# Optimization experiments

Hardware: AMD Instinct MI355X
Metric: run time of the kernel (lower is better)

Reference implementation:

```python
import jax, jax.numpy as jnp
import numpy as np

B, T, D, H, M, CM = 8, 4096, 512, 8, 64, 4
E = D // H          # head dim = 64
F = T // 2 + 1      # rfft length = 2049


def setup_inputs() -> dict:
    key = jax.random.key(0)
    ks = jax.random.split(key, 6)
    scale = 1.0 / (E * E)  # FEDformer weight init: scale * rand
    return {
        "x": jax.random.normal(ks[0], (B, T, D), jnp.float32),
        "Wp": jax.random.normal(ks[1], (D, D), jnp.float32) * (D ** -0.5),
        "bp": jnp.zeros((D,), jnp.float32),
        "w_real": jax.random.uniform(ks[2], (H, E, E, M), jnp.float32) * scale,
        "w_imag": jax.random.uniform(ks[3], (H, E, E, M), jnp.float32) * scale,
        "W1": jax.random.normal(ks[4], (CM * D, D), jnp.float32) * (D ** -0.5),
        "W2": jax.random.normal(ks[5], (D, CM * D), jnp.float32) * ((CM * D) ** -0.5),
        "mode_index": jnp.arange(M, dtype=jnp.int32),  # mode_selection='lowest'
    }


def reference(x, Wp, bp, w_real, w_imag, W1, W2, mode_index):
    b, t, d = x.shape
    # SingleMultiheadProjection: Linear(D, D) then split heads -> [B,T,H,E]
    q = (x @ Wp + bp).reshape(b, t, H, E)
    # FEBf (FourierBlock): permute to [B,H,E,T], rfft over time
    xh = jnp.transpose(q, (0, 2, 3, 1))            # [B,H,E,T]
    x_ft = jnp.fft.rfft(xh, axis=-1)               # [B,H,E,F] complex64
    # sparse mode gather + per-mode complex mixing (bhi,hio->bho per mode)
    xm = jnp.take(x_ft, mode_index, axis=-1)       # [B,H,E,M]
    w = w_real + 1j * w_imag                       # [H,E,E,M]
    om = jnp.einsum('bhim,hiom->bhom', xm, w)      # [B,H,E,M]
    # scatter selected modes back into the zeroed spectrum, inverse transform
    out_ft = jnp.zeros((b, H, E, F), dtype=x_ft.dtype).at[..., mode_index].set(om)
    attn = jnp.fft.irfft(out_ft, n=t, axis=-1)     # [B,H,E,T]
    attn = jnp.transpose(attn, (0, 3, 1, 2)).reshape(b, t, d)
    # residual (dropout=0 / eval mode)
    x = x + attn
    # pointwise-conv FFN: Conv1d(k=1, bias=False) == GEMM over channels
    y = jax.nn.relu(jnp.einsum('btd,cd->btc', x, W1))   # [B,T,CM*D]
    y = jnp.einsum('btc,dc->btd', y, W2)                # [B,T,D]
    return x + y
```

## Files before the change

kernel.cpp:

```cpp
#include <hip/hip_runtime.h>
#include <hip/hip_bf16.h>


#define T_LEN 4096
#define D_MODEL 512
#define NB 8
#define NH 8
#define NE 64
#define NM 64
#define DFF 2048
#define NROWS (NB * T_LEN)
#define NK 128
#define TSPLIT 8
#define TCH (T_LEN / TSPLIT)

typedef __attribute__((ext_vector_type(8))) short bf16x8;
typedef __attribute__((ext_vector_type(4))) float f32x4;

__device__ inline ushort f2bf_rne(float f) {
    unsigned u = __float_as_uint(f);
    unsigned r = u + 0x7FFFu + ((u >> 16) & 1u);
    return (ushort)(r >> 16);
}
__device__ inline float bf2f(ushort h) { return __uint_as_float(((unsigned)h) << 16); }
__device__ inline void split_bf16(float v, ushort& h, ushort& l) {
    h = f2bf_rne(v);
    l = f2bf_rne(v - bf2f(h));
}

#define GLOAD16(gp, lp)                                                            \
    __builtin_amdgcn_global_load_lds(                                              \
        (const __attribute__((address_space(1))) void*)(gp),                       \
        (__attribute__((address_space(3))) void*)(lp), 16, 0, 0)

__global__ __launch_bounds__(256) void basis_kernel(float* __restrict__ basis) {
    int idx = blockIdx.x * 256 + threadIdx.x;
    int t = idx >> 6, m = idx & 63;
    int r = (t * m) & (T_LEN - 1);
    float ang = (float)r * 1.5339807878856412e-3f;
    float s, c;
    sincosf(ang, &s, &c);
    basis[t * 128 + 2 * m]     = c;
    basis[t * 128 + 2 * m + 1] = s;
}

__global__ __launch_bounds__(256) void decomp_kernel(const float* __restrict__ in,
                                                     ushort* __restrict__ hi,
                                                     ushort* __restrict__ lo, int n4) {
    int i = blockIdx.x * 256 + threadIdx.x;
    if (i >= n4) return;
    float4 v = ((const float4*)in)[i];
    ushort4 h, l;
    split_bf16(v.x, h.x, l.x);
    split_bf16(v.y, h.y, l.y);
    split_bf16(v.z, h.z, l.z);
    split_bf16(v.w, h.w, l.w);
    ((ushort4*)hi)[i] = h;
    ((ushort4*)lo)[i] = l;
}

__global__ __launch_bounds__(256) void dft2_kernel(const float* __restrict__ x,
                                                   const float* __restrict__ basis,
                                                   float* __restrict__ pp) {
    __shared__ float xs[64][68];
    __shared__ float bs[64][132];
    int d0 = blockIdx.x * 64;
    int b  = blockIdx.y;
    int tc = blockIdx.z;
    int t0 = tc * TCH;
    int tid = threadIdx.x;
    int tx = tid & 15, ty = tid >> 4;
    float4 acc0[4] = {};
    float4 acc1[4] = {};

    for (int tt = 0; tt < TCH; tt += 64) {
        const float* xrow = x + ((size_t)b * T_LEN + t0 + tt) * D_MODEL + d0;
#pragma unroll
        for (int l = 0; l < 4; ++l) {
            int f = (tid + l * 256) * 4;
            int r = f >> 6, c = f & 63;
            *(float4*)&xs[r][c] = *(const float4*)(xrow + (size_t)r * D_MODEL + c);
        }
        const float* brow = basis + (size_t)(t0 + tt) * NK;
#pragma unroll
        for (int l = 0; l < 8; ++l) {
            int f = (tid + l * 256) * 4;
            int r = f >> 7, c = f & 127;
            *(float4*)&bs[r][c] = *(const float4*)(brow + (size_t)r * NK + c);
        }
        __syncthreads();
#pragma unroll 4
        for (int t = 0; t < 64; ++t) {
            float4 xv = *(const float4*)&xs[t][ty * 4];
            float4 b0 = *(const float4*)&bs[t][tx * 4];
            float4 b1 = *(const float4*)&bs[t][tx * 4 + 64];
            float xa[4] = {xv.x, xv.y, xv.z, xv.w};
#pragma unroll
            for (int di = 0; di < 4; ++di) {
                acc0[di].x = fmaf(xa[di], b0.x, acc0[di].x);
                acc0[di].y = fmaf(xa[di], b0.y, acc0[di].y);
                acc0[di].z = fmaf(xa[di], b0.z, acc0[di].z);
                acc0[di].w = fmaf(xa[di], b0.w, acc0[di].w);
                acc1[di].x = fmaf(xa[di], b1.x, acc1[di].x);
                acc1[di].y = fmaf(xa[di], b1.y, acc1[di].y);
                acc1[di].z = fmaf(xa[di], b1.z, acc1[di].z);
                acc1[di].w = fmaf(xa[di], b1.w, acc1[di].w);
            }
        }
        __syncthreads();
    }
#pragma unroll
    for (int di = 0; di < 4; ++di) {
        int d = d0 + ty * 4 + di;
        size_t base = (((size_t)tc * NB + b) * D_MODEL + d) * NK;
        *(float4*)(pp + base + tx * 4)      = acc0[di];
        *(float4*)(pp + base + 64 + tx * 4) = acc1[di];
    }
}

__global__ __launch_bounds__(256) void dft_reduce_kernel(const float* __restrict__ pp,
                                                         float* __restrict__ Xm) {
    int idx = blockIdx.x * 256 + threadIdx.x;
    const size_t stride = (size_t)NB * D_MODEL * NK;
    float s = 0.f;
#pragma unroll
    for (int tc = 0; tc < TSPLIT; ++tc) s += pp[(size_t)tc * stride + idx];
    Xm[idx] = (idx & 1) ? -s : s;
}

__global__ __launch_bounds__(512) void proj_kernel(const float* __restrict__ Xm,
                                                   const float* __restrict__ Wp,
                                                   const float* __restrict__ bpv,
                                                   float* __restrict__ qm) {
    int m = blockIdx.x, b = blockIdx.y;
    int c = threadIdx.x;
    float qr = 0.f, qi = 0.f;
#pragma unroll 4
    for (int d = 0; d < D_MODEL; ++d) {
        float2 xv = *(const float2*)(Xm + ((size_t)(b * D_MODEL + d) * NM + m) * 2);
        float w = Wp[(size_t)d * D_MODEL + c];
        qr = fmaf(xv.x, w, qr);
        qi = fmaf(xv.y, w, qi);
    }
    if (m == 0) qr += bpv[c] * (float)T_LEN;
    size_t o = ((size_t)(b * D_MODEL + c) * NM + m) * 2;
    qm[o] = qr; qm[o + 1] = qi;
}

__global__ __launch_bounds__(64) void mix_kernel(const float* __restrict__ qm,
                                                 const float* __restrict__ wre,
                                                 const float* __restrict__ wim,
                                                 float* __restrict__ omB) {
    int o = blockIdx.x, h = blockIdx.y, m = threadIdx.x;
    float ar[NB], ai[NB];
#pragma unroll
    for (int b = 0; b < NB; ++b) { ar[b] = 0.f; ai[b] = 0.f; }
    for (int i = 0; i < NE; ++i) {
        size_t wo = (((size_t)(h * NE + i) * NE + o) * NM) + m;
        float wr = wre[wo], wi = wim[wo];
#pragma unroll
        for (int b = 0; b < NB; ++b) {
            float2 q = *(const float2*)(qm + ((size_t)(b * D_MODEL + h * NE + i) * NM + m) * 2);
            ar[b] = fmaf(q.x, wr, fmaf(-q.y, wi, ar[b]));
            ai[b] = fmaf(q.x, wi, fmaf(q.y, wr, ai[b]));
        }
    }
    float cm = (m == 0) ? (1.0f / T_LEN) : (2.0f / T_LEN);
    int cidx = h * NE + o;
#pragma unroll
    for (int b = 0; b < NB; ++b) {
        omB[((size_t)b * 128 + 2 * m) * D_MODEL + cidx]     = ar[b] * cm;
        omB[((size_t)b * 128 + 2 * m + 1) * D_MODEL + cidx] = (m == 0) ? 0.f : -ai[b] * cm;
    }
}

__global__ __launch_bounds__(256) void idft_kernel(const float* __restrict__ x,
                                                   const float* __restrict__ basis,
                                                   const float* __restrict__ omB,
                                                   ushort* __restrict__ xh_hi,
                                                   ushort* __restrict__ xh_lo,
                                                   float* __restrict__ out) {
    __shared__ float bs[64][129];
    __shared__ float os[128][65];
    int b = blockIdx.z;
    int tt = blockIdx.y * 64;
    int dd = blockIdx.x * 64;
    int tid = threadIdx.x;
    for (int i = tid; i < 64 * 128; i += 256) {
        int r = i >> 7, k = i & 127;
        bs[r][k] = basis[(size_t)(tt + r) * 128 + k];
    }
    for (int i = tid; i < 128 * 64; i += 256) {
        int k = i >> 6, dl = i & 63;
        os[k][dl] = omB[((size_t)b * 128 + k) * D_MODEL + dd + dl];
    }
    __syncthreads();
    int tx = tid & 15, ty = tid >> 4;
    int r0 = ty * 4, c0 = tx * 4;
    float acc[4][4] = {};
#pragma unroll 4
    for (int k = 0; k < 128; ++k) {
        float a[4], bv[4];
#pragma unroll
        for (int i = 0; i < 4; ++i) a[i] = bs[r0 + i][k];
#pragma unroll
        for (int j = 0; j < 4; ++j) bv[j] = os[k][c0 + j];
#pragma unroll
        for (int i = 0; i < 4; ++i)
#pragma unroll
            for (int j = 0; j < 4; ++j) acc[i][j] = fmaf(a[i], bv[j], acc[i][j]);
    }
#pragma unroll
    for (int i = 0; i < 4; ++i) {
        size_t off = ((size_t)b * T_LEN + tt + r0 + i) * D_MODEL + dd + c0;
        float4 xv = *(const float4*)(x + off);
        float4 o4;
        o4.x = xv.x + acc[i][0]; o4.y = xv.y + acc[i][1];
        o4.z = xv.z + acc[i][2]; o4.w = xv.w + acc[i][3];
        *(float4*)(out + off) = o4;
        ushort4 hv, lv;
        split_bf16(o4.x, hv.x, lv.x);
        split_bf16(o4.y, hv.y, lv.y);
        split_bf16(o4.z, hv.z, lv.z);
        split_bf16(o4.w, hv.w, lv.w);
        *(ushort4*)(xh_hi + off) = hv;
        *(ushort4*)(xh_lo + off) = lv;
    }
}


__global__ __launch_bounds__(256) void ffn1_mfma(const ushort* __restrict__ Ag_h,
                                                 const ushort* __restrict__ Ag_l,
                                                 const ushort* __restrict__ Bg_h,
                                                 const ushort* __restrict__ Bg_l,
                                                 ushort* __restrict__ Yh,
                                                 ushort* __restrict__ Yl,
                                                 int co, int CH) {
    __shared__ ushort Ah[128][32], Al[128][32], Bh[128][32], Bl[128][32];
    int rr = blockIdx.y * 128;
    int ccl = blockIdx.x * 128;
    int cc = co + ccl;
    int tid = threadIdx.x;
    int lane = tid & 63, w = tid >> 6;
    int wr = (w >> 1) * 64, wc = (w & 1) * 64;
    f32x4 acc[4][4] = {};
    int c0 = w * 2;
    int srow = c0 * 16 + (lane >> 2);
    int koff = (lane & 3) * 8;

    for (int kk = 0; kk < D_MODEL; kk += 32) {
        GLOAD16(Ag_h + (size_t)(rr + srow) * D_MODEL + kk + koff, &Ah[c0 * 16][0]);
        GLOAD16(Ag_h + (size_t)(rr + srow + 16) * D_MODEL + kk + koff, &Ah[c0 * 16 + 16][0]);
        GLOAD16(Ag_l + (size_t)(rr + srow) * D_MODEL + kk + koff, &Al[c0 * 16][0]);
        GLOAD16(Ag_l + (size_t)(rr + srow + 16) * D_MODEL + kk + koff, &Al[c0 * 16 + 16][0]);
        GLOAD16(Bg_h + (size_t)(cc + srow) * D_MODEL + kk + koff, &Bh[c0 * 16][0]);
        GLOAD16(Bg_h + (size_t)(cc + srow + 16) * D_MODEL + kk + koff, &Bh[c0 * 16 + 16][0]);
        GLOAD16(Bg_l + (size_t)(cc + srow) * D_MODEL + kk + koff, &Bl[c0 * 16][0]);
        GLOAD16(Bg_l + (size_t)(cc + srow + 16) * D_MODEL + kk + koff, &Bl[c0 * 16 + 16][0]);
        __syncthreads();
        int arow = wr + (lane & 15);
        int kq = (lane >> 4) * 8;
        bf16x8 afh[4], afl[4];
#pragma unroll
        for (int i = 0; i < 4; ++i) {
            afh[i] = *(const bf16x8*)&Ah[arow + i * 16][kq];
            afl[i] = *(const bf16x8*)&Al[arow + i * 16][kq];
        }
#pragma unroll
        for (int j = 0; j < 4; ++j) {
            int brow = wc + j * 16 + (lane & 15);
            bf16x8 bfh = *(const bf16x8*)&Bh[brow][kq];
            bf16x8 bfl = *(const bf16x8*)&Bl[brow][kq];
#pragma unroll
            for (int i = 0; i < 4; ++i) {
                acc[i][j] = __builtin_amdgcn_mfma_f32_16x16x32_bf16(afh[i], bfh, acc[i][j], 0, 0, 0);
                acc[i][j] = __builtin_amdgcn_mfma_f32_16x16x32_bf16(afl[i], bfh, acc[i][j], 0, 0, 0);
                acc[i][j] = __builtin_amdgcn_mfma_f32_16x16x32_bf16(afh[i], bfl, acc[i][j], 0, 0, 0);
            }
        }
        __syncthreads();
    }
#pragma unroll
    for (int i = 0; i < 4; ++i) {
        int row = rr + wr + i * 16 + (lane >> 4) * 4;
#pragma unroll
        for (int j = 0; j < 4; ++j) {
            int col = ccl + wc + j * 16 + (lane & 15);
#pragma unroll
            for (int q = 0; q < 4; ++q) {
                float v = fmaxf(acc[i][j][q], 0.f);
                ushort h, l;
                split_bf16(v, h, l);
                size_t o = (size_t)(row + q) * CH + col;
                Yh[o] = h;
                Yl[o] = l;
            }
        }
    }
}

__global__ __launch_bounds__(256) void ffn2_mfma(const ushort* __restrict__ Ag_h,
                                                 const ushort* __restrict__ Ag_l,
                                                 const ushort* __restrict__ Bg_h,
                                                 const ushort* __restrict__ Bg_l,
                                                 float* __restrict__ out,
                                                 int co, int CH) {
    __shared__ ushort Ah[128][32], Al[128][32], Bh[128][32], Bl[128][32];
    int rr = blockIdx.y * 128;
    int dd = blockIdx.x * 128;
    int tid = threadIdx.x;
    int lane = tid & 63, w = tid >> 6;
    int wr = (w >> 1) * 64, wc = (w & 1) * 64;
    f32x4 acc[4][4] = {};
    int c0 = w * 2;
    int srow = c0 * 16 + (lane >> 2);
    int koff = (lane & 3) * 8;

    for (int kk = 0; kk < CH; kk += 32) {
        GLOAD16(Ag_h + (size_t)(rr + srow) * CH + kk + koff, &Ah[c0 * 16][0]);
        GLOAD16(Ag_h + (size_t)(rr + srow + 16) * CH + kk + koff, &Ah[c0 * 16 + 16][0]);
        GLOAD16(Ag_l + (size_t)(rr + srow) * CH + kk + koff, &Al[c0 * 16][0]);
        GLOAD16(Ag_l + (size_t)(rr + srow + 16) * CH + kk + koff, &Al[c0 * 16 + 16][0]);
        GLOAD16(Bg_h + (size_t)(dd + srow) * DFF + co + kk + koff, &Bh[c0 * 16][0]);
        GLOAD16(Bg_h + (size_t)(dd + srow + 16) * DFF + co + kk + koff, &Bh[c0 * 16 + 16][0]);
        GLOAD16(Bg_l + (size_t)(dd + srow) * DFF + co + kk + koff, &Bl[c0 * 16][0]);
        GLOAD16(Bg_l + (size_t)(dd + srow + 16) * DFF + co + kk + koff, &Bl[c0 * 16 + 16][0]);
        __syncthreads();
        int arow = wr + (lane & 15);
        int kq = (lane >> 4) * 8;
        bf16x8 afh[4], afl[4];
#pragma unroll
        for (int i = 0; i < 4; ++i) {
            afh[i] = *(const bf16x8*)&Ah[arow + i * 16][kq];
            afl[i] = *(const bf16x8*)&Al[arow + i * 16][kq];
        }
#pragma unroll
        for (int j = 0; j < 4; ++j) {
            int brow = wc + j * 16 + (lane & 15);
            bf16x8 bfh = *(const bf16x8*)&Bh[brow][kq];
            bf16x8 bfl = *(const bf16x8*)&Bl[brow][kq];
#pragma unroll
            for (int i = 0; i < 4; ++i) {
                acc[i][j] = __builtin_amdgcn_mfma_f32_16x16x32_bf16(afh[i], bfh, acc[i][j], 0, 0, 0);
                acc[i][j] = __builtin_amdgcn_mfma_f32_16x16x32_bf16(afl[i], bfh, acc[i][j], 0, 0, 0);
                acc[i][j] = __builtin_amdgcn_mfma_f32_16x16x32_bf16(afh[i], bfl, acc[i][j], 0, 0, 0);
            }
        }
        __syncthreads();
    }
#pragma unroll
    for (int i = 0; i < 4; ++i) {
        int row = rr + wr + i * 16 + (lane >> 4) * 4;
#pragma unroll
        for (int j = 0; j < 4; ++j) {
            int col = dd + wc + j * 16 + (lane & 15);
#pragma unroll
            for (int q = 0; q < 4; ++q) {
                size_t o = (size_t)(row + q) * D_MODEL + col;
                out[o] += acc[i][j][q];
            }
        }
    }
}

extern "C" void kernel_launch(void* const* d_in, const int* in_sizes, int n_in,
                              void* d_out, int out_size, void* d_ws, size_t ws_size,
                              hipStream_t stream) {
    const float* x   = (const float*)d_in[0];
    const float* Wp  = (const float*)d_in[1];
    const float* bpv = (const float*)d_in[2];
    const float* wre = (const float*)d_in[3];
    const float* wim = (const float*)d_in[4];
    const float* W1  = (const float*)d_in[5];
    const float* W2  = (const float*)d_in[6];
    float* out = (float*)d_out;

    char* ws = (char*)d_ws;
    const size_t MB = (size_t)1 << 20;
    float*  basis = (float*)(ws + 0 * MB);
    float*  Xm    = (float*)(ws + 2 * MB);
    float*  qm    = (float*)(ws + 4 * MB);
    float*  omB   = (float*)(ws + 6 * MB);
    ushort* w1h   = (ushort*)(ws + 8 * MB);
    ushort* w1l   = (ushort*)(ws + 10 * MB);
    ushort* w2h   = (ushort*)(ws + 12 * MB);
    ushort* w2l   = (ushort*)(ws + 14 * MB);
    ushort* xh_hi = (ushort*)(ws + 16 * MB);
    ushort* xh_lo = (ushort*)(ws + 48 * MB);
    char*   y1b   = ws + 80 * MB;
    float*  pp    = (float*)(ws + 16 * MB);

    size_t avail = (ws_size > 80 * MB) ? ws_size - 80 * MB : 0;
    int CH = 2048;
    while (CH > 128 && (size_t)NROWS * CH * 2 * sizeof(ushort) > avail) CH >>= 1;
    ushort* y1h = (ushort*)y1b;
    ushort* y1l = (ushort*)(y1b + (size_t)NROWS * CH * sizeof(ushort));

    basis_kernel<<<1024, 256, 0, stream>>>(basis);
    decomp_kernel<<<1024, 256, 0, stream>>>(W1, w1h, w1l, DFF * D_MODEL / 4);
    decomp_kernel<<<1024, 256, 0, stream>>>(W2, w2h, w2l, DFF * D_MODEL / 4);
    dft2_kernel<<<dim3(8, 8, TSPLIT), 256, 0, stream>>>(x, basis, pp);
    dft_reduce_kernel<<<(NB * D_MODEL * NK) / 256, 256, 0, stream>>>(pp, Xm);
    proj_kernel<<<dim3(64, 8), 512, 0, stream>>>(Xm, Wp, bpv, qm);
    mix_kernel<<<dim3(64, 8), 64, 0, stream>>>(qm, wre, wim, omB);
    idft_kernel<<<dim3(8, 64, 8), 256, 0, stream>>>(x, basis, omB, xh_hi, xh_lo, out);
    for (int co = 0; co < DFF; co += CH) {
        ffn1_mfma<<<dim3(CH / 128, NROWS / 128), 256, 0, stream>>>(
            xh_hi, xh_lo, w1h, w1l, y1h, y1l, co, CH);
        ffn2_mfma<<<dim3(D_MODEL / 128, NROWS / 128), 256, 0, stream>>>(
            y1h, y1l, w2h, w2l, out, co, CH);
    }
}
```

Baseline: 869.8 us.

## Rework DFT split, mix/idft parallelism, and FFN GEMM K-step with XCD swizzle

Doubles the time split of the forward DFT and gives the mode-mixing kernel one block per batch, so each thread handles one batch. A transposed basis is added so the inverse-DFT kernel can load tiles with float4 and read them from padded shared memory without strided access. Both FFN MFMA GEMMs now stage 64 K-elements per barrier in a two-slot shared buffer and launch on a 1-D grid whose block index is remapped across the 8 XCDs. The intent is fewer barriers, better L2 locality and higher parallelism in the small kernels. The cost is double the shared memory per GEMM block and an extra 2 MB basis buffer.

```diff
diff --git a/kernel.cpp b/kernel.cpp
--- a/kernel.cpp
+++ b/kernel.cpp
@@ -11,7 +11,7 @@
 #define DFF 2048
 #define NROWS (NB * T_LEN)
 #define NK 128
-#define TSPLIT 8
+#define TSPLIT 16
 #define TCH (T_LEN / TSPLIT)
 
 typedef __attribute__((ext_vector_type(8))) short bf16x8;
@@ -33,15 +33,18 @@
         (const __attribute__((address_space(1))) void*)(gp),                       \
         (__attribute__((address_space(3))) void*)(lp), 16, 0, 0)
 
-__global__ __launch_bounds__(256) void basis_kernel(float* __restrict__ basis) {
+__global__ __launch_bounds__(256) void basis_kernel(float* __restrict__ basis,
+                                                    float* __restrict__ basisT) {
     int idx = blockIdx.x * 256 + threadIdx.x;
-    int t = idx >> 6, m = idx & 63;
+    int k = idx >> 12, t = idx & 4095;
+    int m = k >> 1;
     int r = (t * m) & (T_LEN - 1);
     float ang = (float)r * 1.5339807878856412e-3f;
     float s, c;
     sincosf(ang, &s, &c);
-    basis[t * 128 + 2 * m]     = c;
-    basis[t * 128 + 2 * m + 1] = s;
+    float v = (k & 1) ? s : c;
+    basisT[(size_t)k * T_LEN + t] = v;
+    basis[(size_t)t * NK + k]    = v;
 }
 
 __global__ __launch_bounds__(256) void decomp_kernel(const float* __restrict__ in,
@@ -151,72 +154,63 @@
                                                  const float* __restrict__ wre,
                                                  const float* __restrict__ wim,
                                                  float* __restrict__ omB) {
-    int o = blockIdx.x, h = blockIdx.y, m = threadIdx.x;
-    float ar[NB], ai[NB];
-#pragma unroll
-    for (int b = 0; b < NB; ++b) { ar[b] = 0.f; ai[b] = 0.f; }
+    int o = blockIdx.x, h = blockIdx.y, b = blockIdx.z, m = threadIdx.x;
+    float ar = 0.f, ai = 0.f;
     for (int i = 0; i < NE; ++i) {
         size_t wo = (((size_t)(h * NE + i) * NE + o) * NM) + m;
         float wr = wre[wo], wi = wim[wo];
-#pragma unroll
-        for (int b = 0; b < NB; ++b) {
-            float2 q = *(const float2*)(qm + ((size_t)(b * D_MODEL + h * NE + i) * NM + m) * 2);
-            ar[b] = fmaf(q.x, wr, fmaf(-q.y, wi, ar[b]));
-            ai[b] = fmaf(q.x, wi, fmaf(q.y, wr, ai[b]));
-        }
+        float2 q = *(const float2*)(qm + ((size_t)(b * D_MODEL + h * NE + i) * NM + m) * 2);
+        ar = fmaf(q.x, wr, fmaf(-q.y, wi, ar));
+        ai = fmaf(q.x, wi, fmaf(q.y, wr, ai));
     }
     float cm = (m == 0) ? (1.0f / T_LEN) : (2.0f / T_LEN);
     int cidx = h * NE + o;
-#pragma unroll
-    for (int b = 0; b < NB; ++b) {
-        omB[((size_t)b * 128 + 2 * m) * D_MODEL + cidx]     = ar[b] * cm;
-        omB[((size_t)b * 128 + 2 * m + 1) * D_MODEL + cidx] = (m == 0) ? 0.f : -ai[b] * cm;
-    }
-}
-
-__global__ __launch_bounds__(256) void idft_kernel(const float* __restrict__ x,
-                                                   const float* __restrict__ basis,
-                                                   const float* __restrict__ omB,
-                                                   ushort* __restrict__ xh_hi,
-                                                   ushort* __restrict__ xh_lo,
-                                                   float* __restrict__ out) {
-    __shared__ float bs[64][129];
-    __shared__ float os[128][65];
-    int b = blockIdx.z;
+    omB[((size_t)b * 128 + 2 * m) * D_MODEL + cidx]     = ar * cm;
+    omB[((size_t)b * 128 + 2 * m + 1) * D_MODEL + cidx] = (m == 0) ? 0.f : -ai * cm;
+}
+
+__global__ __launch_bounds__(256) void idft2_kernel(const float* __restrict__ x,
+                                                    const float* __restrict__ basisT,
+                                                    const float* __restrict__ omB,
+                                                    ushort* __restrict__ xh_hi,
+                                                    ushort* __restrict__ xh_lo,
+                                                    float* __restrict__ out) {
+    __shared__ float bT[128][68];
+    __shared__ float os[128][68];
+    int dd = blockIdx.x * 64;
     int tt = blockIdx.y * 64;
-    int dd = blockIdx.x * 64;
+    int b  = blockIdx.z;
     int tid = threadIdx.x;
-    for (int i = tid; i < 64 * 128; i += 256) {
-        int r = i >> 7, k = i & 127;
-        bs[r][k] = basis[(size_t)(tt + r) * 128 + k];
-    }
-    for (int i = tid; i < 128 * 64; i += 256) {
-        int k = i >> 6, dl = i & 63;
-        os[k][dl] = omB[((size_t)b * 128 + k) * D_MODEL + dd + dl];
+#pragma unroll
+    for (int l = 0; l < 8; ++l) {
+        int f = (tid + l * 256) * 4;
+        int r = f >> 6, c = f & 63;
+        *(float4*)&bT[r][c] = *(const float4*)(basisT + (size_t)r * T_LEN + tt + c);
+        *(float4*)&os[r][c] = *(const float4*)(omB + ((size_t)b * NK + r) * D_MODEL + dd + c);
     }
     __syncthreads();
     int tx = tid & 15, ty = tid >> 4;
-    int r0 = ty * 4, c0 = tx * 4;
-    float acc[4][4] = {};
+    float4 acc[4] = {};
 #pragma unroll 4
     for (int k = 0; k < 128; ++k) {
-        float a[4], bv[4];
-#pragma unroll
-        for (int i = 0; i < 4; ++i) a[i] = bs[r0 + i][k];
-#pragma unroll
-        for (int j = 0; j < 4; ++j) bv[j] = os[k][c0 + j];
-#pragma unroll
-        for (int i = 0; i < 4; ++i)
-#pragma unroll
-            for (int j = 0; j < 4; ++j) acc[i][j] = fmaf(a[i], bv[j], acc[i][j]);
+        float4 av = *(const float4*)&bT[k][ty * 4];
+        float4 bv = *(const float4*)&os[k][tx * 4];
+        float aa[4] = {av.x, av.y, av.z, av.w};
+#pragma unroll
+        for (int i = 0; i < 4; ++i) {
+            acc[i].x = fmaf(aa[i], bv.x, acc[i].x);
+            acc[i].y = fmaf(aa[i], bv.y, acc[i].y);
+            acc[i].z = fmaf(aa[i], bv.z, acc[i].z);
+            acc[i].w = fmaf(aa[i], bv.w, acc[i].w);
+        }
     }
 #pragma unroll
     for (int i = 0; i < 4; ++i) {
-        size_t off = ((size_t)b * T_LEN + tt + r0 + i) * D_MODEL + dd + c0;
+        size_t off = ((size_t)b * T_LEN + tt + ty * 4 + i) * D_MODEL + dd + tx * 4;
         float4 xv = *(const float4*)(x + off);
         float4 o4;
-        o4.x = xv.x + acc[i][0]; o4.y = xv.y + acc[i][1];
-        o4.z = xv.z + acc[i][2]; o4.w = xv.w + acc[i][3];
+        o4.x = xv.x + acc[i].x; o4.y = xv.y + acc[i].y;
+        o4.z = xv.z + acc[i].z; o4.w = xv.w + acc[i].w;
         *(float4*)(out + off) = o4;
         ushort4 hv, lv;
         split_bf16(o4.x, hv.x, lv.x);
@@ -235,10 +229,14 @@
                                                  const ushort* __restrict__ Bg_l,
                                                  ushort* __restrict__ Yh,
                                                  ushort* __restrict__ Yl,
-                                                 int co, int CH) {
-    __shared__ ushort Ah[128][32], Al[128][32], Bh[128][32], Bl[128][32];
-    int rr = blockIdx.y * 128;
-    int ccl = blockIdx.x * 128;
+                                                 int co, int CH, int nx) {
+    __shared__ ushort Ah[2][128][32], Al[2][128][32], Bh[2][128][32], Bl[2][128][32];
+    int nwg = gridDim.x;
+    int per = nwg >> 3;
+    int lin = (blockIdx.x & 7) * per + (blockIdx.x >> 3);
+    int bx = lin % nx, by = lin / nx;
+    int rr = by * 128;
+    int ccl = bx * 128;
     int cc = co + ccl;
     int tid = threadIdx.x;
     int lane = tid & 63, w = tid >> 6;
@@ -248,34 +246,41 @@
     int srow = c0 * 16 + (lane >> 2);
     int koff = (lane & 3) * 8;
 
-    for (int kk = 0; kk < D_MODEL; kk += 32) {
-        GLOAD16(Ag_h + (size_t)(rr + srow) * D_MODEL + kk + koff, &Ah[c0 * 16][0]);
-        GLOAD16(Ag_h + (size_t)(rr + srow + 16) * D_MODEL + kk + koff, &Ah[c0 * 16 + 16][0]);
-        GLOAD16(Ag_l + (size_t)(rr + srow) * D_MODEL + kk + koff, &Al[c0 * 16][0]);
-        GLOAD16(Ag_l + (size_t)(rr + srow + 16) * D_MODEL + kk + koff, &Al[c0 * 16 + 16][0]);
-        GLOAD16(Bg_h + (size_t)(cc + srow) * D_MODEL + kk + koff, &Bh[c0 * 16][0]);
-        GLOAD16(Bg_h + (size_t)(cc + srow + 16) * D_MODEL + kk + koff, &Bh[c0 * 16 + 16][0]);
-        GLOAD16(Bg_l + (size_t)(cc + srow) * D_MODEL + kk + koff, &Bl[c0 * 16][0]);
-        GLOAD16(Bg_l + (size_t)(cc + srow + 16) * D_MODEL + kk + koff, &Bl[c0 * 16 + 16][0]);
+    for (int kk = 0; kk < D_MODEL; kk += 64) {
+#pragma unroll
+        for (int h = 0; h < 2; ++h) {
+            int kg = kk + h * 32;
+            GLOAD16(Ag_h + (size_t)(rr + srow) * D_MODEL + kg + koff, &Ah[h][c0 * 16][0]);
+            GLOAD16(Ag_h + (size_t)(rr + srow + 16) * D_MODEL + kg + koff, &Ah[h][c0 * 16 + 16][0]);
+            GLOAD16(Ag_l + (size_t)(rr + srow) * D_MODEL + kg + koff, &Al[h][c0 * 16][0]);
+            GLOAD16(Ag_l + (size_t)(rr + srow + 16) * D_MODEL + kg + koff, &Al[h][c0 * 16 + 16][0]);
+            GLOAD16(Bg_h + (size_t)(cc + srow) * D_MODEL + kg + koff, &Bh[h][c0 * 16][0]);
+            GLOAD16(Bg_h + (size_t)(cc + srow + 16) * D_MODEL + kg + koff, &Bh[h][c0 * 16 + 16][0]);
+            GLOAD16(Bg_l + (size_t)(cc + srow) * D_MODEL + kg + koff, &Bl[h][c0 * 16][0]);
+            GLOAD16(Bg_l + (size_t)(cc + srow + 16) * D_MODEL + kg + koff, &Bl[h][c0 * 16 + 16][0]);
+        }
         __syncthreads();
         int arow = wr + (lane & 15);
         int kq = (lane >> 4) * 8;
-        bf16x8 afh[4], afl[4];
-#pragma unroll
-        for (int i = 0; i < 4; ++i) {
-            afh[i] = *(const bf16x8*)&Ah[arow + i * 16][kq];
-            afl[i] = *(const bf16x8*)&Al[arow + i * 16][kq];
-        }
-#pragma unroll
-        for (int j = 0; j < 4; ++j) {
-            int brow = wc + j * 16 + (lane & 15);
-            bf16x8 bfh = *(const bf16x8*)&Bh[brow][kq];
-            bf16x8 bfl = *(const bf16x8*)&Bl[brow][kq];
+#pragma unroll
+        for (int h = 0; h < 2; ++h) {
+            bf16x8 afh[4], afl[4];
 #pragma unroll
             for (int i = 0; i < 4; ++i) {
-                acc[i][j] = __builtin_amdgcn_mfma_f32_16x16x32_bf16(afh[i], bfh, acc[i][j], 0, 0, 0);
-                acc[i][j] = __builtin_amdgcn_mfma_f32_16x16x32_bf16(afl[i], bfh, acc[i][j], 0, 0, 0);
-                acc[i][j] = __builtin_amdgcn_mfma_f32_16x16x32_bf16(afh[i], bfl, acc[i][j], 0, 0, 0);
+                afh[i] = *(const bf16x8*)&Ah[h][arow + i * 16][kq];
+                afl[i] = *(const bf16x8*)&Al[h][arow + i * 16][kq];
+            }
+#pragma unroll
+            for (int j = 0; j < 4; ++j) {
+                int brow = wc + j * 16 + (lane & 15);
+                bf16x8 bfh = *(const bf16x8*)&Bh[h][brow][kq];
+                bf16x8 bfl = *(const bf16x8*)&Bl[h][brow][kq];
+#pragma unroll
+                for (int i = 0; i < 4; ++i) {
+                    acc[i][j] = __builtin_amdgcn_mfma_f32_16x16x32_bf16(afh[i], bfh, acc[i][j], 0, 0, 0);
+                    acc[i][j] = __builtin_amdgcn_mfma_f32_16x16x32_bf16(afl[i], bfh, acc[i][j], 0, 0, 0);
+                    acc[i][j] = __builtin_amdgcn_mfma_f32_16x16x32_bf16(afh[i], bfl, acc[i][j], 0, 0, 0);
+                }
             }
         }
         __syncthreads();
@@ -305,9 +310,13 @@
                                                  const ushort* __restrict__ Bg_l,
                                                  float* __restrict__ out,
                                                  int co, int CH) {
-    __shared__ ushort Ah[128][32], Al[128][32], Bh[128][32], Bl[128][32];
-    int rr = blockIdx.y * 128;
-    int dd = blockIdx.x * 128;
+    __shared__ ushort Ah[2][128][32], Al[2][128][32], Bh[2][128][32], Bl[2][128][32];
+    int nwg = gridDim.x;
+    int per = nwg >> 3;
+    int lin = (blockIdx.x & 7) * per + (blockIdx.x >> 3);
+    int bx = lin & 3, by = lin >> 2;
+    int rr = by * 128;
+    int dd = bx * 128;
     int tid = threadIdx.x;
     int lane = tid & 63, w = tid >> 6;
     int wr = (w >> 1) * 64, wc = (w & 1) * 64;
@@ -316,34 +325,41 @@
     int srow = c0 * 16 + (lane >> 2);
     int koff = (lane & 3) * 8;
 
-    for (int kk = 0; kk < CH; kk += 32) {
-        GLOAD16(Ag_h + (size_t)(rr + srow) * CH + kk + koff, &Ah[c0 * 16][0]);
-        GLOAD16(Ag_h + (size_t)(rr + srow + 16) * CH + kk + koff, &Ah[c0 * 16 + 16][0]);
-        GLOAD16(Ag_l + (size_t)(rr + srow) * CH + kk + koff, &Al[c0 * 16][0]);
-        GLOAD16(Ag_l + (size_t)(rr + srow + 16) * CH + kk + koff, &Al[c0 * 16 + 16][0]);
-        GLOAD16(Bg_h + (size_t)(dd + srow) * DFF + co + kk + koff, &Bh[c0 * 16][0]);
-        GLOAD16(Bg_h + (size_t)(dd + srow + 16) * DFF + co + kk + koff, &Bh[c0 * 16 + 16][0]);
-        GLOAD16(Bg_l + (size_t)(dd + srow) * DFF + co + kk + koff, &Bl[c0 * 16][0]);
-        GLOAD16(Bg_l + (size_t)(dd + srow + 16) * DFF + co + kk + koff, &Bl[c0 * 16 + 16][0]);
+    for (int kk = 0; kk < CH; kk += 64) {
+#pragma unroll
+        for (int h = 0; h < 2; ++h) {
+            int kg = kk + h * 32;
+            GLOAD16(Ag_h + (size_t)(rr + srow) * CH + kg + koff, &Ah[h][c0 * 16][0]);
+            GLOAD16(Ag_h + (size_t)(rr + srow + 16) * CH + kg + koff, &Ah[h][c0 * 16 + 16][0]);
+            GLOAD16(Ag_l + (size_t)(rr + srow) * CH + kg + koff, &Al[h][c0 * 16][0]);
+            GLOAD16(Ag_l + (size_t)(rr + srow + 16) * CH + kg + koff, &Al[h][c0 * 16 + 16][0]);
+            GLOAD16(Bg_h + (size_t)(dd + srow) * DFF + co + kg + koff, &Bh[h][c0 * 16][0]);
+            GLOAD16(Bg_h + (size_t)(dd + srow + 16) * DFF + co + kg + koff, &Bh[h][c0 * 16 + 16][0]);
+            GLOAD16(Bg_l + (size_t)(dd + srow) * DFF + co + kg + koff, &Bl[h][c0 * 16][0]);
+            GLOAD16(Bg_l + (size_t)(dd + srow + 16) * DFF + co + kg + koff, &Bl[h][c0 * 16 + 16][0]);
+        }
         __syncthreads();
         int arow = wr + (lane & 15);
         int kq = (lane >> 4) * 8;
-        bf16x8 afh[4], afl[4];
-#pragma unroll
-        for (int i = 0; i < 4; ++i) {
-            afh[i] = *(const bf16x8*)&Ah[arow + i * 16][kq];
-            afl[i] = *(const bf16x8*)&Al[arow + i * 16][kq];
-        }
-#pragma unroll
-        for (int j = 0; j < 4; ++j) {
-            int brow = wc + j * 16 + (lane & 15);
-            bf16x8 bfh = *(const bf16x8*)&Bh[brow][kq];
-            bf16x8 bfl = *(const bf16x8*)&Bl[brow][kq];
+#pragma unroll
+        for (int h = 0; h < 2; ++h) {
+            bf16x8 afh[4], afl[4];
 #pragma unroll
             for (int i = 0; i < 4; ++i) {
-                acc[i][j] = __builtin_amdgcn_mfma_f32_16x16x32_bf16(afh[i], bfh, acc[i][j], 0, 0, 0);
-                acc[i][j] = __builtin_amdgcn_mfma_f32_16x16x32_bf16(afl[i], bfh, acc[i][j], 0, 0, 0);
-                acc[i][j] = __builtin_amdgcn_mfma_f32_16x16x32_bf16(afh[i], bfl, acc[i][j], 0, 0, 0);
+                afh[i] = *(const bf16x8*)&Ah[h][arow + i * 16][kq];
+                afl[i] = *(const bf16x8*)&Al[h][arow + i * 16][kq];
+            }
+#pragma unroll
+            for (int j = 0; j < 4; ++j) {
+                int brow = wc + j * 16 + (lane & 15);
+                bf16x8 bfh = *(const bf16x8*)&Bh[h][brow][kq];
+                bf16x8 bfl = *(const bf16x8*)&Bl[h][brow][kq];
+#pragma unroll
+                for (int i = 0; i < 4; ++i) {
+                    acc[i][j] = __builtin_amdgcn_mfma_f32_16x16x32_bf16(afh[i], bfh, acc[i][j], 0, 0, 0);
+                    acc[i][j] = __builtin_amdgcn_mfma_f32_16x16x32_bf16(afl[i], bfh, acc[i][j], 0, 0, 0);
+                    acc[i][j] = __builtin_amdgcn_mfma_f32_16x16x32_bf16(afh[i], bfl, acc[i][j], 0, 0, 0);
+                }
             }
         }
         __syncthreads();
@@ -377,37 +393,39 @@
 
     char* ws = (char*)d_ws;
     const size_t MB = (size_t)1 << 20;
-    float*  basis = (float*)(ws + 0 * MB);
-    float*  Xm    = (float*)(ws + 2 * MB);
-    float*  qm    = (float*)(ws + 4 * MB);
-    float*  omB   = (float*)(ws + 6 * MB);
-    ushort* w1h   = (ushort*)(ws + 8 * MB);
-    ushort* w1l   = (ushort*)(ws + 10 * MB);
-    ushort* w2h   = (ushort*)(ws + 12 * MB);
-    ushort* w2l   = (ushort*)(ws + 14 * MB);
-    ushort* xh_hi = (ushort*)(ws + 16 * MB);
-    ushort* xh_lo = (ushort*)(ws + 48 * MB);
-    char*   y1b   = ws + 80 * MB;
-    float*  pp    = (float*)(ws + 16 * MB);
-
-    size_t avail = (ws_size > 80 * MB) ? ws_size - 80 * MB : 0;
+    float*  basis  = (float*)(ws + 0 * MB);
+    float*  Xm     = (float*)(ws + 2 * MB);
+    float*  qm     = (float*)(ws + 4 * MB);
+    float*  omB    = (float*)(ws + 6 * MB);
+    ushort* w1h    = (ushort*)(ws + 8 * MB);
+    ushort* w1l    = (ushort*)(ws + 10 * MB);
+    ushort* w2h    = (ushort*)(ws + 12 * MB);
+    ushort* w2l    = (ushort*)(ws + 14 * MB);
+    ushort* xh_hi  = (ushort*)(ws + 16 * MB);
+    ushort* xh_lo  = (ushort*)(ws + 48 * MB);
+    float*  basisT = (float*)(ws + 80 * MB);
+    char*   y1b    = ws + 82 * MB;
+    float*  pp     = (float*)(ws + 16 * MB);
+
+    size_t avail = (ws_size > 82 * MB) ? ws_size - 82 * MB : 0;
     int CH = 2048;
     while (CH > 128 && (size_t)NROWS * CH * 2 * sizeof(ushort) > avail) CH >>= 1;
     ushort* y1h = (ushort*)y1b;
     ushort* y1l = (ushort*)(y1b + (size_t)NROWS * CH * sizeof(ushort));
 
-    basis_kernel<<<1024, 256, 0, stream>>>(basis);
+    basis_kernel<<<2048, 256, 0, stream>>>(basis, basisT);
     decomp_kernel<<<1024, 256, 0, stream>>>(W1, w1h, w1l, DFF * D_MODEL / 4);
     decomp_kernel<<<1024, 256, 0, stream>>>(W2, w2h, w2l, DFF * D_MODEL / 4);
     dft2_kernel<<<dim3(8, 8, TSPLIT), 256, 0, stream>>>(x, basis, pp);
     dft_reduce_kernel<<<(NB * D_MODEL * NK) / 256, 256, 0, stream>>>(pp, Xm);
     proj_kernel<<<dim3(64, 8), 512, 0, stream>>>(Xm, Wp, bpv, qm);
-    mix_kernel<<<dim3(64, 8), 64, 0, stream>>>(qm, wre, wim, omB);
-    idft_kernel<<<dim3(8, 64, 8), 256, 0, stream>>>(x, basis, omB, xh_hi, xh_lo, out);
+    mix_kernel<<<dim3(64, 8, 8), 64, 0, stream>>>(qm, wre, wim, omB);
+    idft2_kernel<<<dim3(8, 64, 8), 256, 0, stream>>>(x, basisT, omB, xh_hi, xh_lo, out);
     for (int co = 0; co < DFF; co += CH) {
-        ffn1_mfma<<<dim3(CH / 128, NROWS / 128), 256, 0, stream>>>(
-            xh_hi, xh_lo, w1h, w1l, y1h, y1l, co, CH);
-        ffn2_mfma<<<dim3(D_MODEL / 128, NROWS / 128), 256, 0, stream>>>(
+        int nx = CH / 128;
+        ffn1_mfma<<<nx * 256, 256, 0, stream>>>(
+            xh_hi, xh_lo, w1h, w1l, y1h, y1l, co, CH, nx);
+        ffn2_mfma<<<1024, 256, 0, stream>>>(
             y1h, y1l, w2h, w2l, out, co, CH);
     }
 }
```

New measurement: 817.8 us. 6.0% less time.
